# Performance work log

Measured on AMD Instinct MI355X. Metric: run time of the kernel, lower is better.

Reference implementation:

```python
import jax, jax.numpy as jnp
import numpy as np

B, L, D, H = 2, 2048, 1024, 16
HD = D // H  # head_dim = 64


def _clin(xr, xi, Wr, br, Wi, bi):
    # (x_r + i x_i)(W_r + i W_i): out_r = fc_r(x_r) - fc_i(x_i); out_i = fc_r(x_i) + fc_i(x_r)
    rr = xr @ Wr.T + br
    ii = xi @ Wi.T + bi
    ri = xi @ Wr.T + br
    ir = xr @ Wi.T + bi
    return rr - ii, ri + ir


def _heads(x):
    # [B, L, D] -> [B, H, L, HD]
    return x.reshape(B, L, H, HD).transpose(0, 2, 1, 3)


def setup_inputs() -> dict:
    key = jax.random.key(0)
    ks = jax.random.split(key, 11)
    inp = {
        "x_r": jax.random.normal(ks[0], (B, L, D), jnp.float32),
        "x_i": jax.random.normal(ks[1], (B, L, D), jnp.float32),
        "attention_mask": jnp.zeros((B, 1, 1, L), jnp.float32),
    }
    names = ["Wq_r", "Wq_i", "Wk_r", "Wk_i", "Wv_r", "Wv_i", "Wo_r", "Wo_i"]
    for n, k in zip(names, ks[2:10]):
        inp[n] = jax.random.normal(k, (D, D), jnp.float32) * 0.02
        inp["b" + n[1:]] = jnp.zeros((D,), jnp.float32)
    return inp


def reference(x_r, x_i, attention_mask,
              Wq_r, bq_r, Wq_i, bq_i,
              Wk_r, bk_r, Wk_i, bk_i,
              Wv_r, bv_r, Wv_i, bv_i,
              Wo_r, bo_r, Wo_i, bo_i):
    qr, qi = _clin(x_r, x_i, Wq_r, bq_r, Wq_i, bq_i)
    kr, ki = _clin(x_r, x_i, Wk_r, bk_r, Wk_i, bk_i)
    vr, vi = _clin(x_r, x_i, Wv_r, bv_r, Wv_i, bv_i)
    q_r, q_i = _heads(qr), _heads(qi)
    k_r, k_i = _heads(kr), _heads(ki)
    v_r, v_i = _heads(vr), _heads(vi)
    # complex QK^T cross terms -> squared-magnitude interference score
    s_real = jnp.einsum('bhqd,bhkd->bhqk', q_r, k_r) + jnp.einsum('bhqd,bhkd->bhqk', q_i, k_i)
    s_imag = jnp.einsum('bhqd,bhkd->bhqk', q_i, k_r) - jnp.einsum('bhqd,bhkd->bhqk', q_r, k_i)
    interference = (s_real * s_real + s_imag * s_imag) / HD + attention_mask
    attn = jax.nn.softmax(interference, axis=-1)
    c_r = jnp.einsum('bhqk,bhkd->bhqd', attn, v_r).transpose(0, 2, 1, 3).reshape(B, L, D)
    c_i = jnp.einsum('bhqk,bhkd->bhqd', attn, v_i).transpose(0, 2, 1, 3).reshape(B, L, D)
    out_r, out_i = _clin(c_r, c_i, Wo_r, bo_r, Wo_i, bo_i)
    return out_r, out_i
```

## Files before the change

### kernel.cpp

```cpp
#include <hip/hip_runtime.h>
#include <hip/hip_bf16.h>

typedef unsigned short u16;
typedef __attribute__((ext_vector_type(8))) short bf16x8;
typedef __attribute__((ext_vector_type(8))) _Float16 f16x8;
typedef __attribute__((ext_vector_type(8))) unsigned short u16x8;
typedef __attribute__((ext_vector_type(4))) float f32x4;

__device__ __forceinline__ u16 f2b(float f) {
  _Float16 h = (_Float16)f;
  return __builtin_bit_cast(u16, h);
}

__device__ __forceinline__ f32x4 mfma16(bf16x8 a, bf16x8 b, f32x4 c) {
  return __builtin_amdgcn_mfma_f32_16x16x32_f16(
      __builtin_bit_cast(f16x8, a), __builtin_bit_cast(f16x8, b), c, 0, 0, 0);
}

__device__ __forceinline__ float fexp2(float x) {
  float r; asm("v_exp_f32 %0, %1" : "=v"(r) : "v"(x)); return r;
}

#define GLD16(dst, src) __builtin_amdgcn_global_load_lds( \
    (const __attribute__((address_space(1))) void*)(src), \
    (__attribute__((address_space(3))) void*)(dst), 16, 0, 0)

__global__ void pack_x_kernel(u16* __restrict__ A1, const float* __restrict__ xr,
                              const float* __restrict__ xi) {
  const int id = blockIdx.x * 256 + threadIdx.x;
  const size_t k8 = (size_t)id * 8;
  const int n = (int)(k8 >> 11);
  const int kk = (int)(k8 & 2047);
  const float* src = (kk < 1024) ? (xr + (size_t)n * 1024 + kk)
                                 : (xi + (size_t)n * 1024 + (kk - 1024));
  float4 a = *(const float4*)src;
  float4 c = *(const float4*)(src + 4);
  u16x8 o;
  o[0] = f2b(a.x); o[1] = f2b(a.y); o[2] = f2b(a.z); o[3] = f2b(a.w);
  o[4] = f2b(c.x); o[5] = f2b(c.y); o[6] = f2b(c.z); o[7] = f2b(c.w);
  *(u16x8*)(A1 + k8) = o;
}

struct PWArgs {
  const float* Wr[4]; const float* Wi[4];
  const float* br[4]; const float* bi[4];
};

__global__ void pack_w_all(PWArgs a, int sbase, u16* __restrict__ B1,
                           u16* __restrict__ B2, float* __restrict__ bias1,
                           float* __restrict__ bias2) {
  const int s = sbase + blockIdx.y;
  const int wi = s >> 1, isim = s & 1;
  u16* dst = (s < 6) ? (B1 + (size_t)s * (1024 * 2048))
                     : (B2 + (size_t)(s - 6) * (1024 * 2048));
  float* biasDst = (s < 6) ? (bias1 + s * 1024) : (bias2 + (s - 6) * 1024);
  const int row = blockIdx.x;
  const int kk = threadIdx.x * 8;
  const int half = kk >> 10;
  const int kloc = kk & 1023;
  const float* W = (half == 0) ? (isim ? a.Wi[wi] : a.Wr[wi])
                               : (isim ? a.Wr[wi] : a.Wi[wi]);
  const float sgn = (half == 1 && !isim) ? -1.f : 1.f;
  const float* src = W + (size_t)row * 1024 + kloc;
  float4 x = *(const float4*)src;
  float4 c = *(const float4*)(src + 4);
  u16x8 o;
  o[0] = f2b(sgn * x.x); o[1] = f2b(sgn * x.y); o[2] = f2b(sgn * x.z); o[3] = f2b(sgn * x.w);
  o[4] = f2b(sgn * c.x); o[5] = f2b(sgn * c.y); o[6] = f2b(sgn * c.z); o[7] = f2b(sgn * c.w);
  *(u16x8*)(dst + (size_t)row * 2048 + kk) = o;
  if (threadIdx.x == 0)
    biasDst[row] = isim ? (a.br[wi][row] + a.bi[wi][row])
                        : (a.br[wi][row] - a.bi[wi][row]);
}

template<int MODE>
__global__ __launch_bounds__(256) void gemm_bt(const u16* __restrict__ A,
                                               const u16* __restrict__ Bw,
                                               const float* __restrict__ bias,
                                               void* __restrict__ outp,
                                               u16* __restrict__ vtp) {
  constexpr int K = 2048;
  __shared__ __align__(16) u16 As[128 * 64];
  __shared__ __align__(16) u16 Bs[128 * 64];
  const int tid = threadIdx.x;
  const int w = tid >> 6, l = tid & 63;
  const int l15 = l & 15, lhi = l >> 4;
  const int m0 = blockIdx.y * 128, n0 = blockIdx.x * 128;
  const int wm = w >> 1, wn = w & 1;
  f32x4 acc[4][4] = {};
  for (int kt = 0; kt < K; kt += 64) {
#pragma unroll
    for (int it = 0; it < 4; ++it) {
      const int grp = it * 4 + w;
      const int cl = grp * 64 + l;
      const int r = cl >> 3;
      const int g = (cl & 7) ^ (r & 7);
      GLD16(As + grp * 512, A + (size_t)(m0 + r) * K + kt + g * 8);
      GLD16(Bs + grp * 512, Bw + (size_t)(n0 + r) * K + kt + g * 8);
    }
    __syncthreads();
#pragma unroll
    for (int ks = 0; ks < 2; ++ks) {
      const int c = ks * 4 + lhi;
      bf16x8 af[4], bfr[4];
#pragma unroll
      for (int mf = 0; mf < 4; ++mf) {
        const int r = wm * 64 + mf * 16 + l15;
        af[mf] = *(const bf16x8*)&As[r * 64 + ((c ^ (r & 7)) << 3)];
      }
#pragma unroll
      for (int nf = 0; nf < 4; ++nf) {
        const int r = wn * 64 + nf * 16 + l15;
        bfr[nf] = *(const bf16x8*)&Bs[r * 64 + ((c ^ (r & 7)) << 3)];
      }
#pragma unroll
      for (int mf = 0; mf < 4; ++mf)
#pragma unroll
        for (int nf = 0; nf < 4; ++nf)
          acc[mf][nf] = mfma16(af[mf], bfr[nf], acc[mf][nf]);
    }
    __syncthreads();
  }
#pragma unroll
  for (int nf = 0; nf < 4; ++nf) {
    const int j = n0 + wn * 64 + nf * 16 + l15;
    const float bv = bias[j];
    if constexpr (MODE == 1) {
      const size_t obase = (size_t)(j >> 10) * (4096 * 1024) + (j & 1023);
#pragma unroll
      for (int mf = 0; mf < 4; ++mf)
#pragma unroll
        for (int i = 0; i < 4; ++i) {
          const int row = m0 + wm * 64 + mf * 16 + lhi * 4 + i;
          ((float*)outp)[obase + (size_t)row * 1024] = acc[mf][nf][i] + bv;
        }
    } else {
      if (j < 4096) {
        const size_t obase = (size_t)(j >> 10) * (4096 * 1024) + (j & 1023);
#pragma unroll
        for (int mf = 0; mf < 4; ++mf)
#pragma unroll
          for (int i = 0; i < 4; ++i) {
            const int row = m0 + wm * 64 + mf * 16 + lhi * 4 + i;
            ((u16*)outp)[obase + (size_t)row * 1024] = f2b(acc[mf][nf][i] + bv);
          }
      } else {
        const int jv = j - 4096;
        const size_t vb = (size_t)(jv >> 10) * 4194304 +
                          (size_t)((jv >> 6) & 15) * 131072 +
                          (size_t)(jv & 63) * 2048;
#pragma unroll
        for (int mf = 0; mf < 4; ++mf)
#pragma unroll
          for (int i = 0; i < 4; ++i) {
            const int row = m0 + wm * 64 + mf * 16 + lhi * 4 + i;
            const int b2 = row >> 11, tok = row & 2047;
            vtp[vb + (size_t)b2 * 2097152 + tok] = f2b(acc[mf][nf][i] + bv);
          }
      }
    }
  }
}

__global__ __launch_bounds__(256, 4) void attn_kernel(const u16* __restrict__ qkv,
                                                      const u16* __restrict__ vt,
                                                      const float* __restrict__ mask,
                                                      u16* __restrict__ A2) {
  __shared__ __align__(16) u16 KVb[2][4][2048];
  __shared__ __align__(16) u16 Pl[4][16 * 40];
  const int tid = threadIdx.x, w = tid >> 6, l = tid & 63;
  const int l15 = l & 15, lhi = l >> 4;
  const int q0 = blockIdx.x * 64;
  const int bh = blockIdx.y;
  const int b = bh >> 4, h = bh & 15;
  const size_t M1 = (size_t)4096 * 1024;
  const u16* qr_b = qkv;
  const u16* qi_b = qkv + M1;
  const u16* kr_b = qkv + 2 * M1;
  const u16* ki_b = qkv + 3 * M1;
  const u16* vtr = vt;
  const u16* vti = vt + (size_t)32 * 64 * 2048;
  constexpr float LOG2E = 1.4426950408889634f;
  constexpr float C2 = 0.015625f * LOG2E;

  const size_t qrow = (size_t)(b * 2048 + q0 + w * 16 + l15) * 1024 + h * 64;
  bf16x8 qr[2], qi[2], qrn[2];
#pragma unroll
  for (int ks = 0; ks < 2; ++ks) {
    qr[ks] = *(const bf16x8*)&qr_b[qrow + ks * 32 + lhi * 8];
    qi[ks] = *(const bf16x8*)&qi_b[qrow + ks * 32 + lhi * 8];
    qrn[ks] = qr[ks] ^ (short)0x8000;
  }
  float mrow[4], srow[4];
  f32x4 o_r[4] = {}, o_i[4] = {};
#pragma unroll
  for (int i = 0; i < 4; ++i) { mrow[i] = -1e30f; srow[i] = 0.f; }
  u16* Pw = Pl[w];

  auto STAGE = [&](int tile, int bufi) {
    const int k0s = tile * 32;
    if (w < 2) {
      const u16* src = w ? ki_b : kr_b;
      u16* dstb = &KVb[bufi][w][0];
#pragma unroll
      for (int it = 0; it < 4; ++it) {
        const int cl = it * 64 + l;
        const int r = cl >> 3;
        const int g = (cl & 7) ^ (r & 7);
        GLD16(dstb + it * 512, src + (size_t)(b * 2048 + k0s + r) * 1024 + h * 64 + g * 8);
      }
    } else {
      const u16* src = (w == 3) ? vti : vtr;
      u16* dstb = &KVb[bufi][w][0];
#pragma unroll
      for (int it = 0; it < 4; ++it) {
        const int cl = it * 64 + l;
        const int r = cl >> 2;
        const int g = (cl & 3) ^ ((r >> 1) & 3);
        GLD16(dstb + it * 512, src + (size_t)(bh * 64 + r) * 2048 + k0s + g * 8);
      }
    }
  };

  STAGE(0, 0);
#pragma unroll 2
  for (int kt = 0; kt < 64; ++kt) {
    const int cur = kt & 1;
    const int k0 = kt * 32;
    __syncthreads();
    if (kt < 63) STAGE(kt + 1, cur ^ 1);
    const u16* Kr = &KVb[cur][0][0];
    const u16* Ki = &KVb[cur][1][0];
    const u16* Vr = &KVb[cur][2][0];
    const u16* Vi = &KVb[cur][3][0];
    f32x4 sr[2] = {}, si[2] = {};
    __builtin_amdgcn_s_setprio(1);
#pragma unroll
    for (int nf = 0; nf < 2; ++nf) {
      const int rk = nf * 16 + l15;
      const int sw = rk & 7;
#pragma unroll
      for (int ks = 0; ks < 2; ++ks) {
        const int c = ks * 4 + lhi;
        const int off = rk * 64 + ((c ^ sw) << 3);
        bf16x8 kfr = *(const bf16x8*)&Kr[off];
        bf16x8 kfi = *(const bf16x8*)&Ki[off];
        sr[nf] = mfma16(qr[ks], kfr, sr[nf]);
        sr[nf] = mfma16(qi[ks], kfi, sr[nf]);
        si[nf] = mfma16(qi[ks], kfr, si[nf]);
        si[nf] = mfma16(qrn[ks], kfi, si[nf]);
      }
    }
    __builtin_amdgcn_s_setprio(0);
    float t[2][4];
#pragma unroll
    for (int nf = 0; nf < 2; ++nf) {
      const float mkl = mask[b * 2048 + k0 + nf * 16 + l15] * LOG2E;
#pragma unroll
      for (int i = 0; i < 4; ++i) {
        const float ss = fmaf(si[nf][i], si[nf][i], sr[nf][i] * sr[nf][i]);
        t[nf][i] = fmaf(ss, C2, mkl);
      }
    }
    float pmax[4];
#pragma unroll
    for (int i = 0; i < 4; ++i) {
      float v = fmaxf(t[0][i], t[1][i]);
      v = fmaxf(v, __shfl_xor(v, 1, 64));
      v = fmaxf(v, __shfl_xor(v, 2, 64));
      v = fmaxf(v, __shfl_xor(v, 4, 64));
      v = fmaxf(v, __shfl_xor(v, 8, 64));
      pmax[i] = v;
    }
    bool grow = false;
#pragma unroll
    for (int i = 0; i < 4; ++i) grow |= (pmax[i] > mrow[i] + 11.f);
    if (__any(grow)) {
#pragma unroll
      for (int i = 0; i < 4; ++i) {
        const float mn = fmaxf(mrow[i], pmax[i]);
        const float sc = fexp2(mrow[i] - mn);
        mrow[i] = mn;
        srow[i] *= sc;
#pragma unroll
        for (int nf = 0; nf < 4; ++nf) { o_r[nf][i] *= sc; o_i[nf][i] *= sc; }
      }
    }
    float p[2][4];
#pragma unroll
    for (int nf = 0; nf < 2; ++nf)
#pragma unroll
      for (int i = 0; i < 4; ++i) {
        p[nf][i] = fexp2(t[nf][i] - mrow[i]);
        srow[i] += p[nf][i];
      }
#pragma unroll
    for (int nf = 0; nf < 2; ++nf)
#pragma unroll
      for (int i = 0; i < 4; ++i)
        Pw[(lhi * 4 + i) * 40 + nf * 16 + l15] = f2b(p[nf][i]);
    bf16x8 pa = *(const bf16x8*)&Pw[l15 * 40 + lhi * 8];
    __builtin_amdgcn_s_setprio(1);
#pragma unroll
    for (int nf = 0; nf < 4; ++nf) {
      const int d = nf * 16 + l15;
      const int off = d * 32 + ((lhi ^ ((d >> 1) & 3)) << 3);
      bf16x8 vfr = *(const bf16x8*)&Vr[off];
      bf16x8 vfi = *(const bf16x8*)&Vi[off];
      o_r[nf] = mfma16(pa, vfr, o_r[nf]);
      o_i[nf] = mfma16(pa, vfi, o_i[nf]);
    }
    __builtin_amdgcn_s_setprio(0);
  }
  float inv[4];
#pragma unroll
  for (int i = 0; i < 4; ++i) {
    float v = srow[i];
    v += __shfl_xor(v, 1, 64);
    v += __shfl_xor(v, 2, 64);
    v += __shfl_xor(v, 4, 64);
    v += __shfl_xor(v, 8, 64);
    inv[i] = 1.f / v;
  }
  const int rowbase = b * 2048 + q0 + w * 16 + lhi * 4;
#pragma unroll
  for (int nf = 0; nf < 4; ++nf) {
    const int col = h * 64 + nf * 16 + l15;
#pragma unroll
    for (int i = 0; i < 4; ++i) {
      const size_t rw = (size_t)(rowbase + i) * 2048;
      A2[rw + col] = f2b(o_r[nf][i] * inv[i]);
      A2[rw + 1024 + col] = f2b(o_i[nf][i] * inv[i]);
    }
  }
}

extern "C" void kernel_launch(void* const* d_in, const int* in_sizes, int n_in,
                              void* d_out, int out_size, void* d_ws, size_t ws_size,
                              hipStream_t stream) {
  (void)in_sizes; (void)n_in; (void)out_size; (void)ws_size;
  const float* x_r  = (const float*)d_in[0];
  const float* x_i  = (const float*)d_in[1];
  const float* mask = (const float*)d_in[2];

  PWArgs pw;
  pw.Wr[0] = (const float*)d_in[3];  pw.br[0] = (const float*)d_in[4];
  pw.Wi[0] = (const float*)d_in[5];  pw.bi[0] = (const float*)d_in[6];
  pw.Wr[1] = (const float*)d_in[7];  pw.br[1] = (const float*)d_in[8];
  pw.Wi[1] = (const float*)d_in[9];  pw.bi[1] = (const float*)d_in[10];
  pw.Wr[2] = (const float*)d_in[11]; pw.br[2] = (const float*)d_in[12];
  pw.Wi[2] = (const float*)d_in[13]; pw.bi[2] = (const float*)d_in[14];
  pw.Wr[3] = (const float*)d_in[15]; pw.br[3] = (const float*)d_in[16];
  pw.Wi[3] = (const float*)d_in[17]; pw.bi[3] = (const float*)d_in[18];

  char* ws = (char*)d_ws;
  u16* A     = (u16*)(ws);
  u16* B1    = (u16*)(ws + (16u << 20));
  u16* B2    = (u16*)(ws + (16u << 20));
  u16* qkvp  = (u16*)(ws + (40u << 20));
  u16* vtp   = (u16*)(ws + (72u << 20));
  float* bias1 = (float*)(ws + (88u << 20));
  float* bias2 = (float*)(ws + (88u << 20) + (1u << 15));

  pack_x_kernel<<<4096, 256, 0, stream>>>(A, x_r, x_i);
  pack_w_all<<<dim3(1024, 6), 256, 0, stream>>>(pw, 0, B1, B2, bias1, bias2);

  gemm_bt<0><<<dim3(48, 32), 256, 0, stream>>>(A, B1, bias1, qkvp, vtp);

  pack_w_all<<<dim3(1024, 2), 256, 0, stream>>>(pw, 6, B1, B2, bias1, bias2);

  attn_kernel<<<dim3(32, 32), 256, 0, stream>>>(qkvp, vtp, mask, A);

  gemm_bt<1><<<dim3(16, 32), 256, 0, stream>>>(A, B2, bias2, d_out, nullptr);
}
```

Baseline: 486.5 us.

## Rewrite attention with 32x32 MFMA, transposed scores, register P and LDS mask

The attention kernel now computes S^T with 32x32x16 MFMA tiles, so each wave owns 32 queries and each lane holds a single query's softmax state. The row max comes from in-register reduction plus one cross-half shuffle, and the P fragment is built by packing and shuffling registers rather than bouncing through LDS. The mask is preloaded into shared memory once per block. Each block covers 128 queries, so the grid halves and launch bounds drop to 2 blocks per CU, which trades occupancy for more work per wave and fewer K/V reloads.

```diff
diff --git a/kernel.cpp b/kernel.cpp
--- a/kernel.cpp
+++ b/kernel.cpp
@@ -4,8 +4,10 @@
 typedef unsigned short u16;
 typedef __attribute__((ext_vector_type(8))) short bf16x8;
 typedef __attribute__((ext_vector_type(8))) _Float16 f16x8;
+typedef __attribute__((ext_vector_type(2))) _Float16 f16x2;
 typedef __attribute__((ext_vector_type(8))) unsigned short u16x8;
 typedef __attribute__((ext_vector_type(4))) float f32x4;
+typedef __attribute__((ext_vector_type(16))) float f32x16;
 
 __device__ __forceinline__ u16 f2b(float f) {
   _Float16 h = (_Float16)f;
@@ -14,6 +16,11 @@
 
 __device__ __forceinline__ f32x4 mfma16(bf16x8 a, bf16x8 b, f32x4 c) {
   return __builtin_amdgcn_mfma_f32_16x16x32_f16(
+      __builtin_bit_cast(f16x8, a), __builtin_bit_cast(f16x8, b), c, 0, 0, 0);
+}
+
+__device__ __forceinline__ f32x16 mfma32(bf16x8 a, bf16x8 b, f32x16 c) {
+  return __builtin_amdgcn_mfma_f32_32x32x16_f16(
       __builtin_bit_cast(f16x8, a), __builtin_bit_cast(f16x8, b), c, 0, 0, 0);
 }
 
@@ -162,15 +169,15 @@
   }
 }
 
-__global__ __launch_bounds__(256, 4) void attn_kernel(const u16* __restrict__ qkv,
+__global__ __launch_bounds__(256, 2) void attn_kernel(const u16* __restrict__ qkv,
                                                       const u16* __restrict__ vt,
                                                       const float* __restrict__ mask,
                                                       u16* __restrict__ A2) {
   __shared__ __align__(16) u16 KVb[2][4][2048];
-  __shared__ __align__(16) u16 Pl[4][16 * 40];
+  __shared__ float maskL[2048];
   const int tid = threadIdx.x, w = tid >> 6, l = tid & 63;
-  const int l15 = l & 15, lhi = l >> 4;
-  const int q0 = blockIdx.x * 64;
+  const int tok = l & 31, hi = l >> 5;
+  const int q0 = blockIdx.x * 128;
   const int bh = blockIdx.y;
   const int b = bh >> 4, h = bh & 15;
   const size_t M1 = (size_t)4096 * 1024;
@@ -183,19 +190,25 @@
   constexpr float LOG2E = 1.4426950408889634f;
   constexpr float C2 = 0.015625f * LOG2E;
 
-  const size_t qrow = (size_t)(b * 2048 + q0 + w * 16 + l15) * 1024 + h * 64;
-  bf16x8 qr[2], qi[2], qrn[2];
-#pragma unroll
-  for (int ks = 0; ks < 2; ++ks) {
-    qr[ks] = *(const bf16x8*)&qr_b[qrow + ks * 32 + lhi * 8];
-    qi[ks] = *(const bf16x8*)&qi_b[qrow + ks * 32 + lhi * 8];
+  {
+    const float4* msrc = (const float4*)(mask + (size_t)b * 2048);
+    float4 m0 = msrc[tid * 2], m1 = msrc[tid * 2 + 1];
+    float4 s0 = {m0.x * LOG2E, m0.y * LOG2E, m0.z * LOG2E, m0.w * LOG2E};
+    float4 s1 = {m1.x * LOG2E, m1.y * LOG2E, m1.z * LOG2E, m1.w * LOG2E};
+    *(float4*)&maskL[tid * 8] = s0;
+    *(float4*)&maskL[tid * 8 + 4] = s1;
+  }
+
+  const size_t qrow = (size_t)(b * 2048 + q0 + w * 32 + tok) * 1024 + h * 64 + hi * 8;
+  bf16x8 qr[4], qi[4], qrn[4];
+#pragma unroll
+  for (int ks = 0; ks < 4; ++ks) {
+    qr[ks] = *(const bf16x8*)&qr_b[qrow + ks * 16];
+    qi[ks] = *(const bf16x8*)&qi_b[qrow + ks * 16];
     qrn[ks] = qr[ks] ^ (short)0x8000;
   }
-  float mrow[4], srow[4];
-  f32x4 o_r[4] = {}, o_i[4] = {};
-#pragma unroll
-  for (int i = 0; i < 4; ++i) { mrow[i] = -1e30f; srow[i] = 0.f; }
-  u16* Pw = Pl[w];
+  float mrow = -1e30f, srow = 0.f;
+  f32x16 o_r[2] = {}, o_i[2] = {};
 
   auto STAGE = [&](int tile, int bufi) {
     const int k0s = tile * 32;
@@ -221,6 +234,9 @@
       }
     }
   };
+
+  const int krow = tok * 64;
+  const int ksw = tok & 7;
 
   STAGE(0, 0);
 #pragma unroll 2
@@ -233,104 +249,97 @@
     const u16* Ki = &KVb[cur][1][0];
     const u16* Vr = &KVb[cur][2][0];
     const u16* Vi = &KVb[cur][3][0];
-    f32x4 sr[2] = {}, si[2] = {};
+    f32x16 sr = {}, si = {};
     __builtin_amdgcn_s_setprio(1);
 #pragma unroll
+    for (int ks = 0; ks < 4; ++ks) {
+      const int off = krow + (((ks * 2 + hi) ^ ksw) << 3);
+      bf16x8 kfr = *(const bf16x8*)&Kr[off];
+      bf16x8 kfi = *(const bf16x8*)&Ki[off];
+      sr = mfma32(kfr, qr[ks], sr);
+      sr = mfma32(kfi, qi[ks], sr);
+      si = mfma32(kfr, qi[ks], si);
+      si = mfma32(kfi, qrn[ks], si);
+    }
+    __builtin_amdgcn_s_setprio(0);
+    float t[16];
+#pragma unroll
+    for (int qd = 0; qd < 4; ++qd) {
+      const float4 mk = *(const float4*)&maskL[k0 + qd * 8 + hi * 4];
+#pragma unroll
+      for (int j = 0; j < 4; ++j) {
+        const int r = qd * 4 + j;
+        const float ss = fmaf(si[r], si[r], sr[r] * sr[r]);
+        t[r] = fmaf(ss, C2, ((const float*)&mk)[j]);
+      }
+    }
+    float pmax = t[0];
+#pragma unroll
+    for (int r = 1; r < 16; ++r) pmax = fmaxf(pmax, t[r]);
+    pmax = fmaxf(pmax, __shfl_xor(pmax, 32, 64));
+    if (__any(pmax > mrow + 11.f)) {
+      const float mn = fmaxf(mrow, pmax);
+      const float sc = fexp2(mrow - mn);
+      mrow = mn;
+      srow *= sc;
+#pragma unroll
+      for (int r = 0; r < 16; ++r) {
+        const float scr = __shfl(sc, (r & 3) + 8 * (r >> 2) + 4 * hi, 64);
+        o_r[0][r] *= scr; o_r[1][r] *= scr;
+        o_i[0][r] *= scr; o_i[1][r] *= scr;
+      }
+    }
+    float p[16];
+#pragma unroll
+    for (int r = 0; r < 16; ++r) {
+      p[r] = fexp2(t[r] - mrow);
+      srow += p[r];
+    }
+    unsigned P[8];
+#pragma unroll
+    for (int e = 0; e < 8; ++e)
+      P[e] = __builtin_bit_cast(unsigned,
+               __builtin_amdgcn_cvt_pkrtz(p[2 * e], p[2 * e + 1]));
+    const bool h0 = (hi == 0);
+    const unsigned r0 = (unsigned)__shfl_xor((int)(h0 ? P[2] : P[0]), 32, 64);
+    const unsigned r1 = (unsigned)__shfl_xor((int)(h0 ? P[3] : P[1]), 32, 64);
+    const unsigned r2 = (unsigned)__shfl_xor((int)(h0 ? P[6] : P[4]), 32, 64);
+    const unsigned r3 = (unsigned)__shfl_xor((int)(h0 ? P[7] : P[5]), 32, 64);
+    unsigned fa0[4] = { h0 ? P[0] : r0, h0 ? P[1] : r1, h0 ? r0 : P[2], h0 ? r1 : P[3] };
+    unsigned fa1[4] = { h0 ? P[4] : r2, h0 ? P[5] : r3, h0 ? r2 : P[6], h0 ? r3 : P[7] };
+    bf16x8 pa0, pa1;
+#pragma unroll
+    for (int e = 0; e < 4; ++e) {
+      ((unsigned*)&pa0)[e] = fa0[e];
+      ((unsigned*)&pa1)[e] = fa1[e];
+    }
+    __builtin_amdgcn_s_setprio(1);
+#pragma unroll
     for (int nf = 0; nf < 2; ++nf) {
-      const int rk = nf * 16 + l15;
-      const int sw = rk & 7;
-#pragma unroll
-      for (int ks = 0; ks < 2; ++ks) {
-        const int c = ks * 4 + lhi;
-        const int off = rk * 64 + ((c ^ sw) << 3);
-        bf16x8 kfr = *(const bf16x8*)&Kr[off];
-        bf16x8 kfi = *(const bf16x8*)&Ki[off];
-        sr[nf] = mfma16(qr[ks], kfr, sr[nf]);
-        sr[nf] = mfma16(qi[ks], kfi, sr[nf]);
-        si[nf] = mfma16(qi[ks], kfr, si[nf]);
-        si[nf] = mfma16(qrn[ks], kfi, si[nf]);
-      }
+      const int dv = nf * 32 + tok;
+      const int vsw = (dv >> 1) & 3;
+      const int voff0 = dv * 32 + ((hi ^ vsw) << 3);
+      const int voff1 = dv * 32 + (((2 + hi) ^ vsw) << 3);
+      o_r[nf] = mfma32(pa0, *(const bf16x8*)&Vr[voff0], o_r[nf]);
+      o_i[nf] = mfma32(pa0, *(const bf16x8*)&Vi[voff0], o_i[nf]);
+      o_r[nf] = mfma32(pa1, *(const bf16x8*)&Vr[voff1], o_r[nf]);
+      o_i[nf] = mfma32(pa1, *(const bf16x8*)&Vi[voff1], o_i[nf]);
     }
     __builtin_amdgcn_s_setprio(0);
-    float t[2][4];
+  }
+  const float stot = srow + __shfl_xor(srow, 32, 64);
+  const float invq = 1.f / stot;
+  const int rowbase = b * 2048 + q0 + w * 32;
+#pragma unroll
+  for (int r = 0; r < 16; ++r) {
+    const int qr2 = (r & 3) + 8 * (r >> 2) + 4 * hi;
+    const float iv = __shfl(invq, qr2, 64);
+    const size_t rw = (size_t)(rowbase + qr2) * 2048;
 #pragma unroll
     for (int nf = 0; nf < 2; ++nf) {
-      const float mkl = mask[b * 2048 + k0 + nf * 16 + l15] * LOG2E;
-#pragma unroll
-      for (int i = 0; i < 4; ++i) {
-        const float ss = fmaf(si[nf][i], si[nf][i], sr[nf][i] * sr[nf][i]);
-        t[nf][i] = fmaf(ss, C2, mkl);
-      }
-    }
-    float pmax[4];
-#pragma unroll
-    for (int i = 0; i < 4; ++i) {
-      float v = fmaxf(t[0][i], t[1][i]);
-      v = fmaxf(v, __shfl_xor(v, 1, 64));
-      v = fmaxf(v, __shfl_xor(v, 2, 64));
-      v = fmaxf(v, __shfl_xor(v, 4, 64));
-      v = fmaxf(v, __shfl_xor(v, 8, 64));
-      pmax[i] = v;
-    }
-    bool grow = false;
-#pragma unroll
-    for (int i = 0; i < 4; ++i) grow |= (pmax[i] > mrow[i] + 11.f);
-    if (__any(grow)) {
-#pragma unroll
-      for (int i = 0; i < 4; ++i) {
-        const float mn = fmaxf(mrow[i], pmax[i]);
-        const float sc = fexp2(mrow[i] - mn);
-        mrow[i] = mn;
-        srow[i] *= sc;
-#pragma unroll
-        for (int nf = 0; nf < 4; ++nf) { o_r[nf][i] *= sc; o_i[nf][i] *= sc; }
-      }
-    }
-    float p[2][4];
-#pragma unroll
-    for (int nf = 0; nf < 2; ++nf)
-#pragma unroll
-      for (int i = 0; i < 4; ++i) {
-        p[nf][i] = fexp2(t[nf][i] - mrow[i]);
-        srow[i] += p[nf][i];
-      }
-#pragma unroll
-    for (int nf = 0; nf < 2; ++nf)
-#pragma unroll
-      for (int i = 0; i < 4; ++i)
-        Pw[(lhi * 4 + i) * 40 + nf * 16 + l15] = f2b(p[nf][i]);
-    bf16x8 pa = *(const bf16x8*)&Pw[l15 * 40 + lhi * 8];
-    __builtin_amdgcn_s_setprio(1);
-#pragma unroll
-    for (int nf = 0; nf < 4; ++nf) {
-      const int d = nf * 16 + l15;
-      const int off = d * 32 + ((lhi ^ ((d >> 1) & 3)) << 3);
-      bf16x8 vfr = *(const bf16x8*)&Vr[off];
-      bf16x8 vfi = *(const bf16x8*)&Vi[off];
-      o_r[nf] = mfma16(pa, vfr, o_r[nf]);
-      o_i[nf] = mfma16(pa, vfi, o_i[nf]);
-    }
-    __builtin_amdgcn_s_setprio(0);
-  }
-  float inv[4];
-#pragma unroll
-  for (int i = 0; i < 4; ++i) {
-    float v = srow[i];
-    v += __shfl_xor(v, 1, 64);
-    v += __shfl_xor(v, 2, 64);
-    v += __shfl_xor(v, 4, 64);
-    v += __shfl_xor(v, 8, 64);
-    inv[i] = 1.f / v;
-  }
-  const int rowbase = b * 2048 + q0 + w * 16 + lhi * 4;
-#pragma unroll
-  for (int nf = 0; nf < 4; ++nf) {
-    const int col = h * 64 + nf * 16 + l15;
-#pragma unroll
-    for (int i = 0; i < 4; ++i) {
-      const size_t rw = (size_t)(rowbase + i) * 2048;
-      A2[rw + col] = f2b(o_r[nf][i] * inv[i]);
-      A2[rw + 1024 + col] = f2b(o_i[nf][i] * inv[i]);
+      const int col = h * 64 + nf * 32 + tok;
+      A2[rw + col] = f2b(o_r[nf][r] * iv);
+      A2[rw + 1024 + col] = f2b(o_i[nf][r] * iv);
     }
   }
 }
@@ -369,7 +378,7 @@
 
   pack_w_all<<<dim3(1024, 2), 256, 0, stream>>>(pw, 6, B1, B2, bias1, bias2);
 
-  attn_kernel<<<dim3(32, 32), 256, 0, stream>>>(qkvp, vtp, mask, A);
+  attn_kernel<<<dim3(16, 32), 256, 0, stream>>>(qkvp, vtp, mask, A);
 
   gemm_bt<1><<<dim3(16, 32), 256, 0, stream>>>(A, B2, bias2, d_out, nullptr);
 }
```

New measurement: 422.5 us. 1.15x faster.
